# Optimization experiments

Hardware: AMD Instinct MI355X
Metric: run time of the kernel (lower is better)

## Reference

```python
import jax, jax.numpy as jnp
import numpy as np

B, T, D, H, DH, W = 2, 2048, 512, 8, 64, 64  # batch, seq, d_model, heads, d_head, window
BASE = 10000.0


def rope(x):
    # x: [b, t, d]; rotate-half RoPE applied over the full feature dim (as in source: pos_enc on d_model)
    d = x.shape[-1]
    half = d // 2
    inv_freq = BASE ** (-jnp.arange(half, dtype=jnp.float32) / half)          # [half]
    ang = jnp.arange(x.shape[1], dtype=jnp.float32)[:, None] * inv_freq       # [t, half]
    cos, sin = jnp.cos(ang), jnp.sin(ang)
    x1, x2 = x[..., :half], x[..., half:]
    return jnp.concatenate([x1 * cos - x2 * sin, x1 * sin + x2 * cos], axis=-1)


def setup_inputs() -> dict:
    key = jax.random.key(0)
    k0, k1, k2, k3 = jax.random.split(key, 4)
    x = jax.random.normal(k0, (B, T, D), jnp.float32)
    Wq = jax.random.normal(k1, (D, D), jnp.float32) / jnp.sqrt(D)
    Wkv = jax.random.normal(k2, (D, 2 * D), jnp.float32) / jnp.sqrt(D)
    # NOTE: source zero-inits lin; we use random weights so the output/grads are non-trivial
    Wlin = jax.random.normal(k3, (D, D), jnp.float32) / jnp.sqrt(D)
    blin = jnp.zeros((D,), jnp.float32)
    return {"x": x, "Wq": Wq, "Wkv": Wkv, "Wlin": Wlin, "blin": blin}


def reference(x, Wq, Wkv, Wlin, blin):
    b, t, _ = x.shape
    scale = DH ** -0.5
    q = rope(x @ Wq).reshape(b, t, H, DH).transpose(0, 2, 1, 3)               # [b,h,t,d]
    kv = x @ Wkv
    k, v = kv[..., :D], kv[..., D:]
    k = rope(k).reshape(b, t, H, DH).transpose(0, 2, 1, 3)                    # [b,h,t,d]
    v = v.reshape(b, t, H, DH).transpose(0, 2, 1, 3)                          # [b,h,t,d]
    pad = [(0, 0), (0, 0), (W - 1, 0), (0, 0)]
    kp, vp = jnp.pad(k, pad), jnp.pad(v, pad)                                 # [b,h,t+W-1,d]
    idx = jnp.arange(t)[:, None] + jnp.arange(W)[None, :]                     # [t,W] sliding-window gather
    kw, vw = kp[:, :, idx], vp[:, :, idx]                                     # [b,h,t,W,d]
    attn = jax.nn.softmax(jnp.einsum('bhtd,bhtwd->bhtw', q, kw) * scale, axis=-1)
    out = jnp.einsum('bhtw,bhtwd->bhtd', attn, vw)                            # [b,h,t,d]
    out = out.transpose(0, 2, 1, 3).reshape(b, t, D)
    return out @ Wlin + blin
```

## Files before the change

### kernel.cpp

```cpp
#include <hip/hip_runtime.h>
#include <cstddef>

#define T_N 2048
#define M_N 4096
#define KW  512

typedef __attribute__((ext_vector_type(4))) float f32x4;
typedef _Float16 f16x8 __attribute__((ext_vector_type(8)));
typedef _Float16 f16x4 __attribute__((ext_vector_type(4)));
typedef _Float16 f16x2 __attribute__((ext_vector_type(2)));

#define GLOAD_LDS(g, l) __builtin_amdgcn_global_load_lds( \
    (const __attribute__((address_space(1))) unsigned int*)(g), \
    (__attribute__((address_space(3))) unsigned int*)(l), 16, 0, 0)

__global__ __launch_bounds__(256) void prep(
    const float* __restrict__ x, const float* __restrict__ Wq,
    const float* __restrict__ Wkv, const float* __restrict__ Wlin,
    _Float16* __restrict__ Axp, _Float16* __restrict__ Wcatp,
    _Float16* __restrict__ Wlinp, _Float16* __restrict__ tab16) {
  __shared__ float tile[64][65];
  const int bid = blockIdx.x;
  const int tid = threadIdx.x;
  if (bid < 1024) {
    int idx = bid * 256 + tid;
    int m = idx >> 6, k8 = (idx & 63) << 3;
    const float* src = x + (size_t)m * 512 + k8;
    const float4 a = *(const float4*)src;
    const float4 b = *(const float4*)(src + 4);
    f16x8 o;
    o[0] = (_Float16)a.x; o[1] = (_Float16)a.y; o[2] = (_Float16)a.z; o[3] = (_Float16)a.w;
    o[4] = (_Float16)b.x; o[5] = (_Float16)b.y; o[6] = (_Float16)b.z; o[7] = (_Float16)b.w;
    *(f16x8*)(Axp + (size_t)m * 512 + k8) = o;
    return;
  }
  if (bid >= 1280) {
    int gid = (bid - 1280) * 256 + tid;
    int t = gid >> 8, f = gid & 255;
    float invf = exp2f(-0.05190512648261503f * (float)f);
    float s, c;
    sincosf((float)t * invf, &s, &c);
    f16x2 cs;
    cs[0] = (_Float16)c; cs[1] = (_Float16)s;
    *(f16x2*)(tab16 + 2 * ((size_t)t * 256 + f)) = cs;
    return;
  }
  int wb = bid - 1024;
  const float* W; int N; int mode; int bx, by;
  if (wb < 64)       { W = Wq;   N = 512;  mode = 0; bx = wb & 7;  by = wb >> 3; }
  else if (wb < 192) { wb -= 64;  W = Wkv; N = 1024; mode = 1; bx = wb & 15; by = wb >> 4; }
  else               { wb -= 192; W = Wlin; N = 512; mode = 2; bx = wb & 7;  by = wb >> 3; }
  const int n0 = bx * 64, k0 = by * 64;
#pragma unroll
  for (int it = 0; it < 16; ++it) {
    int idx = tid + it * 256;
    int r = idx >> 6, c = idx & 63;
    tile[r][c] = W[(size_t)(k0 + r) * N + n0 + c];
  }
  __syncthreads();
#pragma unroll
  for (int it = 0; it < 16; ++it) {
    int idx = tid + it * 256;
    int n = idx >> 6, kk = idx & 63;
    int cg = n0 + n;
    int np; _Float16* out;
    if (mode == 0)      { np = 2 * (cg & 255) + (cg >> 8); out = Wcatp; }
    else if (mode == 1) { np = (cg < 512) ? 512 + 2 * (cg & 255) + (cg >> 8)
                                          : 1024 + (cg - 512);
                          out = Wcatp; }
    else                { np = cg; out = Wlinp; }
    out[(size_t)np * KW + k0 + kk] = (_Float16)tile[kk][n];
  }
}

__global__ __launch_bounds__(256) void gemm_qkv_rope(
    const _Float16* __restrict__ Ap, const _Float16* __restrict__ Bp,
    const _Float16* __restrict__ tab16, _Float16* __restrict__ Qh,
    _Float16* __restrict__ Kh, _Float16* __restrict__ Vh) {
  __shared__ __align__(16) _Float16 sm[64 * 64 + 128 * 64];
  _Float16* sA = sm;
  _Float16* sB = sm + 64 * 64;
  const int tid = threadIdx.x;
  const int wid = tid >> 6, lane = tid & 63;
  const int il = lane & 15, g = lane >> 4;
  const int m0 = blockIdx.y * 64, n0 = blockIdx.x * 128;
  const int wm = (wid >> 1) * 32, wn = (wid & 1) * 64;
  f32x4 acc[2][4] = {};

  const _Float16* ga = Ap + (size_t)(m0 + wid * 16 + (lane >> 3)) * KW + (lane & 7) * 8;
  const _Float16* gb = Bp + (size_t)(n0 + wid * 32 + (lane >> 3)) * KW + (lane & 7) * 8;
  _Float16* la = sA + wid * 16 * 64;
  _Float16* lb = sB + wid * 32 * 64;

  for (int k0 = 0; k0 < KW; k0 += 64) {
    GLOAD_LDS(ga + k0, la);
    GLOAD_LDS(ga + 8 * KW + k0, la + 8 * 64);
#pragma unroll
    for (int p = 0; p < 4; ++p)
      GLOAD_LDS(gb + (size_t)(p * 8) * KW + k0, lb + p * 8 * 64);
    __syncthreads();
#pragma unroll
    for (int ks = 0; ks < 2; ++ks) {
      f16x8 af[2], bf[4];
#pragma unroll
      for (int i = 0; i < 2; ++i)
        af[i] = *(const f16x8*)&sA[(wm + i * 16 + il) * 64 + ks * 32 + g * 8];
#pragma unroll
      for (int j = 0; j < 4; ++j)
        bf[j] = *(const f16x8*)&sB[(wn + j * 16 + il) * 64 + ks * 32 + g * 8];
#pragma unroll
      for (int i = 0; i < 2; ++i)
#pragma unroll
        for (int j = 0; j < 4; ++j)
          acc[i][j] = __builtin_amdgcn_mfma_f32_16x16x32_f16(af[i], bf[j], acc[i][j], 0, 0, 0);
    }
    __syncthreads();
  }
  const int b8 = (m0 >> 11) * 8;
  const int tb = m0 & (T_N - 1);
  const bool isv = (n0 >= 1024);
  const bool isk = (n0 >= 512) && !isv;
  _Float16* OT  = sm;
  _Float16* OTV = sm;

  if (isv) {
#pragma unroll
    for (int i = 0; i < 2; ++i)
#pragma unroll
      for (int j = 0; j < 4; ++j) {
        f32x4 v = acc[i][j];
        int col = wn + 16 * j + il;
#pragma unroll
        for (int r = 0; r < 4; ++r) {
          int tl = wm + i * 16 + g * 4 + r;
          OTV[col * 72 + tl] = (_Float16)v[r];
        }
      }
    __syncthreads();
    const int cv = n0 - 1024;
#pragma unroll
    for (int it = 0; it < 4; ++it) {
      int c = tid + it * 256;
      int col = c >> 3, t8 = (c & 7) * 8;
      int h = (cv + col) >> 6, d = (cv + col) & 63;
      *(f16x8*)(Vh + ((size_t)(b8 + h) * 64 + d) * T_N + tb + t8) =
          *(const f16x8*)&OTV[col * 72 + t8];
    }
    return;
  }
  const int n0p = n0 - (isk ? 512 : 0);
  const int h0 = n0p >> 7;
#pragma unroll
  for (int i = 0; i < 2; ++i) {
#pragma unroll
    for (int j = 0; j < 4; ++j) {
      f32x4 v = acc[i][j];
#pragma unroll
      for (int r = 0; r < 4; ++r) {
        float self = v[r];
        float part = __shfl_xor(self, 1);
        int tl = wm + i * 16 + g * 4 + r;
        int tpos = tb + tl;
        int p = il & 1;
        int f = (n0p + wn + 16 * j + (il & 14)) >> 1;
        f16x2 cs = *(const f16x2*)(tab16 + 2 * ((size_t)tpos * 256 + f));
        float c = (float)cs[0], s = (float)cs[1];
        float o = p ? (self * c + part * s) : (self * c - part * s);
        OT[(p * 64 + tl) * 72 + (f & 63)] = (_Float16)o;
      }
    }
  }
  __syncthreads();
  _Float16* dst = isk ? Kh : Qh;
#pragma unroll
  for (int it = 0; it < 4; ++it) {
    int c = tid + it * 256;
    int p = c >> 9, row = (c >> 3) & 63, d8 = (c & 7) * 8;
    *(f16x8*)(dst + ((size_t)(b8 + h0 + 4 * p) * T_N + tb + row) * 64 + d8) =
        *(const f16x8*)&OT[(p * 64 + row) * 72 + d8];
  }
}

__global__ __launch_bounds__(256, 2) void attn_fused(
    const _Float16* __restrict__ Qh, const _Float16* __restrict__ Kh,
    const _Float16* __restrict__ Vh, _Float16* __restrict__ Aout) {
  __shared__ __align__(16) _Float16 sm[31232];
  _Float16* Ks  = sm;
  _Float16* VTs = sm + 9216;
  _Float16* Qs  = sm + 17920;
  _Float16* Ps  = sm + 22528;
  _Float16* OH  = sm;

  const int wgid = blockIdx.x;
  const int orig = (wgid & 7) * 64 + (wgid >> 3);
  const int tile = orig & 31;
  const int h = (orig >> 5) & 7;
  const int b = orig >> 8;
  const int t0 = tile * 64;
  const int tid = threadIdx.x;
  const size_t bh = (size_t)(b * 8 + h);

#pragma unroll
  for (int itn = 0; itn < 2; ++itn) {
    int c = tid + itn * 256;
    int row = c >> 3, d8 = (c & 7) * 8;
    *(f16x8*)(Qs + row * 72 + d8) =
        *(const f16x8*)(Qh + (bh * T_N + t0 + row) * 64 + d8);
  }
#pragma unroll
  for (int itn = 0; itn < 4; ++itn) {
    int c = tid + itn * 256;
    int jr = c >> 3, d8 = (c & 7) * 8;
    int p = t0 - 64 + jr;
    f16x8 o = {};
    if (p >= 0) o = *(const f16x8*)(Kh + (bh * T_N + p) * 64 + d8);
    *(f16x8*)(Ks + jr * 72 + d8) = o;
  }
#pragma unroll
  for (int itn = 0; itn < 4; ++itn) {
    int c = tid + itn * 256;
    int d = c & 63, jr8 = (c >> 6) * 8;
    int p8 = t0 - 64 + jr8;
    f16x8 o = {};
    if (p8 >= 0) o = *(const f16x8*)(Vh + (bh * 64 + d) * T_N + p8);
    *(f16x8*)(VTs + d * 136 + jr8) = o;
  }
  __syncthreads();

  const int lane = tid & 63;
  const int il = lane & 15, g = lane >> 4;
  const int it = tid >> 6;
  const int i_q = 16 * it + il;

  f32x4 sacc[5] = {};
  {
    f16x8 qf0 = *(const f16x8*)(Qs + i_q * 72 + 8 * g);
    f16x8 qf1 = *(const f16x8*)(Qs + i_q * 72 + 32 + 8 * g);
#pragma unroll
    for (int jt5 = 0; jt5 < 5; ++jt5) {
      int jrow = 16 * (it + jt5) + il;
      f16x8 a0 = *(const f16x8*)(Ks + jrow * 72 + 8 * g);
      f16x8 a1 = *(const f16x8*)(Ks + jrow * 72 + 32 + 8 * g);
      sacc[jt5] = __builtin_amdgcn_mfma_f32_16x16x32_f16(a0, qf0, sacc[jt5], 0, 0, 0);
      sacc[jt5] = __builtin_amdgcn_mfma_f32_16x16x32_f16(a1, qf1, sacc[jt5], 0, 0, 0);
    }
  }
  float mx = -3e38f;
#pragma unroll
  for (int jt5 = 0; jt5 < 5; ++jt5)
#pragma unroll
    for (int r = 0; r < 4; ++r) {
      int j = 16 * (it + jt5) + 4 * g + r;
      int wv = j - 1 - i_q;
      if (wv >= 0 && wv < 64) mx = fmaxf(mx, sacc[jt5][r]);
    }
  mx = fmaxf(mx, __shfl_xor(mx, 16));
  mx = fmaxf(mx, __shfl_xor(mx, 32));
  float sum = 0.f;
#pragma unroll
  for (int jt5 = 0; jt5 < 5; ++jt5) {
    f16x4 pv;
#pragma unroll
    for (int r = 0; r < 4; ++r) {
      int j = 16 * (it + jt5) + 4 * g + r;
      int wv = j - 1 - i_q;
      float ex = 0.f;
      if (wv >= 0 && wv < 64) {
        ex = exp2f((sacc[jt5][r] - mx) * 0.18033688011112042f);
        sum += ex;
      }
      pv[r] = (_Float16)ex;
    }
    *(f16x4*)(Ps + i_q * 136 + 16 * (it + jt5) + 4 * g) = pv;
  }
  sum += __shfl_xor(sum, 16);
  sum += __shfl_xor(sum, 32);
  {
    int jtz = (it & 1) ? (it - 1) : (it + 5);
    f16x4 z = {};
    *(f16x4*)(Ps + i_q * 136 + 16 * jtz + 4 * g) = z;
  }

  const int jb = 32 * (it >> 1);
  f32x4 oacc[4] = {};
#pragma unroll
  for (int ks = 0; ks < 3; ++ks) {
    f16x8 pf = *(const f16x8*)(Ps + i_q * 136 + jb + 32 * ks + 8 * g);
#pragma unroll
    for (int dt = 0; dt < 4; ++dt) {
      f16x8 vf = *(const f16x8*)(VTs + (16 * dt + il) * 136 + jb + 32 * ks + 8 * g);
      oacc[dt] = __builtin_amdgcn_mfma_f32_16x16x32_f16(pf, vf, oacc[dt], 0, 0, 0);
    }
  }
  __syncthreads();
#pragma unroll
  for (int r = 0; r < 4; ++r) {
    float s4 = __shfl(sum, 4 * g + r);
    float inv = 1.f / s4;
    int i = 16 * it + 4 * g + r;
#pragma unroll
    for (int dt = 0; dt < 4; ++dt) {
      int d = 16 * dt + il;
      OH[i * 72 + d] = (_Float16)(oacc[dt][r] * inv);
    }
  }
  __syncthreads();
#pragma unroll
  for (int itn = 0; itn < 2; ++itn) {
    int c = tid + itn * 256;
    int row = c >> 3, d8 = (c & 7) * 8;
    *(f16x8*)(Aout + ((size_t)(b * T_N + t0 + row)) * 512 + h * 64 + d8) =
        *(const f16x8*)(OH + row * 72 + d8);
  }
}

__global__ __launch_bounds__(256) void gemm_out(
    const _Float16* __restrict__ Ap, const _Float16* __restrict__ Bp,
    const float* __restrict__ bias, float* __restrict__ C) {
  __shared__ __align__(16) _Float16 sA[64 * 64];
  __shared__ __align__(16) _Float16 sB[64 * 64];
  const int tid = threadIdx.x;
  const int wid = tid >> 6, lane = tid & 63;
  const int il = lane & 15, g = lane >> 4;
  const int m0 = blockIdx.y * 64, n0 = blockIdx.x * 64;
  const int wm = (wid >> 1) * 32, wn = (wid & 1) * 32;
  f32x4 acc[2][2] = {};

  const _Float16* ga = Ap + (size_t)(m0 + wid * 16 + (lane >> 3)) * KW + (lane & 7) * 8;
  const _Float16* gb = Bp + (size_t)(n0 + wid * 16 + (lane >> 3)) * KW + (lane & 7) * 8;
  _Float16* la = sA + wid * 16 * 64;
  _Float16* lb = sB + wid * 16 * 64;

  for (int k0 = 0; k0 < KW; k0 += 64) {
    GLOAD_LDS(ga + k0, la);
    GLOAD_LDS(ga + 8 * KW + k0, la + 8 * 64);
    GLOAD_LDS(gb + k0, lb);
    GLOAD_LDS(gb + 8 * KW + k0, lb + 8 * 64);
    __syncthreads();
#pragma unroll
    for (int ks = 0; ks < 2; ++ks) {
      f16x8 af[2], bf[2];
#pragma unroll
      for (int i = 0; i < 2; ++i)
        af[i] = *(const f16x8*)&sA[(wm + i * 16 + il) * 64 + ks * 32 + g * 8];
#pragma unroll
      for (int j = 0; j < 2; ++j)
        bf[j] = *(const f16x8*)&sB[(wn + j * 16 + il) * 64 + ks * 32 + g * 8];
#pragma unroll
      for (int i = 0; i < 2; ++i)
#pragma unroll
        for (int j = 0; j < 2; ++j)
          acc[i][j] = __builtin_amdgcn_mfma_f32_16x16x32_f16(af[i], bf[j], acc[i][j], 0, 0, 0);
    }
    __syncthreads();
  }
  const int cn = n0 + wn + il;
  const int rbase = m0 + wm + g * 4;
#pragma unroll
  for (int j = 0; j < 2; ++j) {
    float badd = bias[cn + j * 16];
#pragma unroll
    for (int i = 0; i < 2; ++i)
#pragma unroll
      for (int r = 0; r < 4; ++r)
        C[(size_t)(rbase + i * 16 + r) * 512 + cn + j * 16] = acc[i][j][r] + badd;
  }
}

extern "C" void kernel_launch(void* const* d_in, const int* in_sizes, int n_in,
                              void* d_out, int out_size, void* d_ws, size_t ws_size,
                              hipStream_t stream) {
  const float* x    = (const float*)d_in[0];
  const float* Wq   = (const float*)d_in[1];
  const float* Wkv  = (const float*)d_in[2];
  const float* Wlin = (const float*)d_in[3];
  const float* blin = (const float*)d_in[4];
  float* out = (float*)d_out;

  char* ws = (char*)d_ws;
  _Float16* Axp   = (_Float16*)(ws);
  _Float16* Wcatp = (_Float16*)(ws + 4194304);
  _Float16* Wlinp = (_Float16*)(ws + 5767168);
  _Float16* tab16 = (_Float16*)(ws + 6291456);
  _Float16* Qh    = (_Float16*)(ws + 8388608);
  _Float16* Kh    = (_Float16*)(ws + 12582912);
  _Float16* Vh    = (_Float16*)(ws + 16777216);
  _Float16* Aaop  = (_Float16*)(ws + 20971520);

  prep<<<3328, 256, 0, stream>>>(x, Wq, Wkv, Wlin, Axp, Wcatp, Wlinp, tab16);
  gemm_qkv_rope<<<dim3(12, 64), 256, 0, stream>>>(Axp, Wcatp, tab16, Qh, Kh, Vh);
  attn_fused<<<512, 256, 0, stream>>>(Qh, Kh, Vh, Aaop);
  gemm_out<<<dim3(8, 64), 256, 0, stream>>>(Aaop, Wlinp, blin, out);
}
```

Before: 104.1 us.

## Fuse all four kernels into one persistent kernel with grid barriers

Merges the prep, QKV GEMM+RoPE, sliding-window attention and output GEMM kernels into a single 512-block persistent kernel. The stages are separated by software grid barriers built on atomic counters, and the counters are reset with a memset before each launch. This is meant to remove the launch overhead and inter-kernel gaps between the four stages. The cost is spin-wait barriers, a fixed 512-block grid that must all be co-resident or the kernel deadlocks, and a QKV GEMM stage that now spreads 768 tiles unevenly over 512 blocks.

After: 272.5 us. 162% more time.

```diff
diff --git a/kernel.cpp b/kernel.cpp
--- a/kernel.cpp
+++ b/kernel.cpp
@@ -4,6 +4,7 @@
 #define T_N 2048
 #define M_N 4096
 #define KW  512
+#define NBLK 512
 
 typedef __attribute__((ext_vector_type(4))) float f32x4;
 typedef _Float16 f16x8 __attribute__((ext_vector_type(8)));
@@ -14,356 +15,372 @@
     (const __attribute__((address_space(1))) unsigned int*)(g), \
     (__attribute__((address_space(3))) unsigned int*)(l), 16, 0, 0)
 
-__global__ __launch_bounds__(256) void prep(
+__device__ __forceinline__ void gridbar(unsigned* cnt) {
+  __syncthreads();
+  if (threadIdx.x == 0) {
+    __threadfence();
+    __hip_atomic_fetch_add(cnt, 1u, __ATOMIC_ACQ_REL, __HIP_MEMORY_SCOPE_AGENT);
+    while (__hip_atomic_load(cnt, __ATOMIC_ACQUIRE, __HIP_MEMORY_SCOPE_AGENT) < NBLK)
+      __builtin_amdgcn_s_sleep(2);
+    __threadfence();
+  }
+  __syncthreads();
+}
+
+__global__ __launch_bounds__(256, 2) void fused_all(
     const float* __restrict__ x, const float* __restrict__ Wq,
     const float* __restrict__ Wkv, const float* __restrict__ Wlin,
+    const float* __restrict__ blin, float* __restrict__ Cout,
     _Float16* __restrict__ Axp, _Float16* __restrict__ Wcatp,
-    _Float16* __restrict__ Wlinp, _Float16* __restrict__ tab16) {
-  __shared__ float tile[64][65];
+    _Float16* __restrict__ Wlinp, _Float16* __restrict__ tab16,
+    _Float16* __restrict__ Qh, _Float16* __restrict__ Kh,
+    _Float16* __restrict__ Vh, _Float16* __restrict__ Aaop,
+    unsigned* __restrict__ bar) {
+  __shared__ __align__(16) char smraw[62464];
   const int bid = blockIdx.x;
   const int tid = threadIdx.x;
-  if (bid < 1024) {
-    int idx = bid * 256 + tid;
-    int m = idx >> 6, k8 = (idx & 63) << 3;
-    const float* src = x + (size_t)m * 512 + k8;
-    const float4 a = *(const float4*)src;
-    const float4 b = *(const float4*)(src + 4);
-    f16x8 o;
-    o[0] = (_Float16)a.x; o[1] = (_Float16)a.y; o[2] = (_Float16)a.z; o[3] = (_Float16)a.w;
-    o[4] = (_Float16)b.x; o[5] = (_Float16)b.y; o[6] = (_Float16)b.z; o[7] = (_Float16)b.w;
-    *(f16x8*)(Axp + (size_t)m * 512 + k8) = o;
-    return;
+
+  {
+#pragma unroll
+    for (int itn = 0; itn < 2; ++itn) {
+      int idx = bid * 512 + itn * 256 + tid;
+      int m = idx >> 6, k8 = (idx & 63) << 3;
+      const float* src = x + (size_t)m * 512 + k8;
+      const float4 a = *(const float4*)src;
+      const float4 b = *(const float4*)(src + 4);
+      f16x8 o;
+      o[0] = (_Float16)a.x; o[1] = (_Float16)a.y; o[2] = (_Float16)a.z; o[3] = (_Float16)a.w;
+      o[4] = (_Float16)b.x; o[5] = (_Float16)b.y; o[6] = (_Float16)b.z; o[7] = (_Float16)b.w;
+      *(f16x8*)(Axp + (size_t)m * 512 + k8) = o;
+    }
+    if (bid < 256) {
+      float (*tile)[65] = (float(*)[65])smraw;
+      int wb = bid;
+      const float* W; int N; int mode; int bx, by;
+      if (wb < 64)       { W = Wq;   N = 512;  mode = 0; bx = wb & 7;  by = wb >> 3; }
+      else if (wb < 192) { wb -= 64;  W = Wkv; N = 1024; mode = 1; bx = wb & 15; by = wb >> 4; }
+      else               { wb -= 192; W = Wlin; N = 512; mode = 2; bx = wb & 7;  by = wb >> 3; }
+      const int n0 = bx * 64, k0 = by * 64;
+#pragma unroll
+      for (int itn = 0; itn < 16; ++itn) {
+        int idx = tid + itn * 256;
+        int r = idx >> 6, c = idx & 63;
+        tile[r][c] = W[(size_t)(k0 + r) * N + n0 + c];
+      }
+      __syncthreads();
+#pragma unroll
+      for (int itn = 0; itn < 16; ++itn) {
+        int idx = tid + itn * 256;
+        int n = idx >> 6, kk = idx & 63;
+        int cg = n0 + n;
+        int np; _Float16* outp;
+        if (mode == 0)      { np = 2 * (cg & 255) + (cg >> 8); outp = Wcatp; }
+        else if (mode == 1) { np = (cg < 512) ? 512 + 2 * (cg & 255) + (cg >> 8)
+                                              : 1024 + (cg - 512);
+                              outp = Wcatp; }
+        else                { np = cg; outp = Wlinp; }
+        outp[(size_t)np * KW + k0 + kk] = (_Float16)tile[kk][n];
+      }
+    } else {
+#pragma unroll
+      for (int itn = 0; itn < 8; ++itn) {
+        int gid = (bid - 256) * 2048 + itn * 256 + tid;
+        int t = gid >> 8, f = gid & 255;
+        float invf = exp2f(-0.05190512648261503f * (float)f);
+        float s, c;
+        sincosf((float)t * invf, &s, &c);
+        f16x2 cs;
+        cs[0] = (_Float16)c; cs[1] = (_Float16)s;
+        *(f16x2*)(tab16 + 2 * ((size_t)t * 256 + f)) = cs;
+      }
+    }
   }
-  if (bid >= 1280) {
-    int gid = (bid - 1280) * 256 + tid;
-    int t = gid >> 8, f = gid & 255;
-    float invf = exp2f(-0.05190512648261503f * (float)f);
-    float s, c;
-    sincosf((float)t * invf, &s, &c);
-    f16x2 cs;
-    cs[0] = (_Float16)c; cs[1] = (_Float16)s;
-    *(f16x2*)(tab16 + 2 * ((size_t)t * 256 + f)) = cs;
-    return;
+  gridbar(bar + 0);
+
+  for (int tt = bid; tt < 768; tt += NBLK) {
+    __syncthreads();
+    _Float16* sA = (_Float16*)smraw;
+    _Float16* sB = (_Float16*)smraw + 64 * 64;
+    const int wid = tid >> 6, lane = tid & 63;
+    const int il = lane & 15, g = lane >> 4;
+    const int m0 = (tt & 63) * 64, n0 = (tt >> 6) * 128;
+    const int wm = (wid >> 1) * 32, wn = (wid & 1) * 64;
+    f32x4 acc[2][4] = {};
+
+    const _Float16* ga = Axp + (size_t)(m0 + wid * 16 + (lane >> 3)) * KW + (lane & 7) * 8;
+    const _Float16* gb = Wcatp + (size_t)(n0 + wid * 32 + (lane >> 3)) * KW + (lane & 7) * 8;
+    _Float16* la = sA + wid * 16 * 64;
+    _Float16* lb = sB + wid * 32 * 64;
+
+    for (int k0 = 0; k0 < KW; k0 += 64) {
+      GLOAD_LDS(ga + k0, la);
+      GLOAD_LDS(ga + 8 * KW + k0, la + 8 * 64);
+#pragma unroll
+      for (int p = 0; p < 4; ++p)
+        GLOAD_LDS(gb + (size_t)(p * 8) * KW + k0, lb + p * 8 * 64);
+      __syncthreads();
+#pragma unroll
+      for (int ks = 0; ks < 2; ++ks) {
+        f16x8 af[2], bf[4];
+#pragma unroll
+        for (int i = 0; i < 2; ++i)
+          af[i] = *(const f16x8*)&sA[(wm + i * 16 + il) * 64 + ks * 32 + g * 8];
+#pragma unroll
+        for (int j = 0; j < 4; ++j)
+          bf[j] = *(const f16x8*)&sB[(wn + j * 16 + il) * 64 + ks * 32 + g * 8];
+#pragma unroll
+        for (int i = 0; i < 2; ++i)
+#pragma unroll
+          for (int j = 0; j < 4; ++j)
+            acc[i][j] = __builtin_amdgcn_mfma_f32_16x16x32_f16(af[i], bf[j], acc[i][j], 0, 0, 0);
+      }
+      __syncthreads();
+    }
+    const int b8 = (m0 >> 11) * 8;
+    const int tb = m0 & (T_N - 1);
+    const bool isv = (n0 >= 1024);
+    const bool isk = (n0 >= 512) && !isv;
+    _Float16* OT  = (_Float16*)smraw;
+    _Float16* OTV = (_Float16*)smraw;
+
+    if (isv) {
+#pragma unroll
+      for (int i = 0; i < 2; ++i)
+#pragma unroll
+        for (int j = 0; j < 4; ++j) {
+          f32x4 v = acc[i][j];
+          int col = wn + 16 * j + il;
+#pragma unroll
+          for (int r = 0; r < 4; ++r) {
+            int tl = wm + i * 16 + g * 4 + r;
+            OTV[col * 72 + tl] = (_Float16)v[r];
+          }
+        }
+      __syncthreads();
+      const int cv = n0 - 1024;
+#pragma unroll
+      for (int itn = 0; itn < 4; ++itn) {
+        int c = tid + itn * 256;
+        int col = c >> 3, t8 = (c & 7) * 8;
+        int h = (cv + col) >> 6, d = (cv + col) & 63;
+        *(f16x8*)(Vh + ((size_t)(b8 + h) * 64 + d) * T_N + tb + t8) =
+            *(const f16x8*)&OTV[col * 72 + t8];
+      }
+    } else {
+      const int n0p = n0 - (isk ? 512 : 0);
+      const int h0 = n0p >> 7;
+#pragma unroll
+      for (int i = 0; i < 2; ++i) {
+#pragma unroll
+        for (int j = 0; j < 4; ++j) {
+          f32x4 v = acc[i][j];
+#pragma unroll
+          for (int r = 0; r < 4; ++r) {
+            float self = v[r];
+            float part = __shfl_xor(self, 1);
+            int tl = wm + i * 16 + g * 4 + r;
+            int tpos = tb + tl;
+            int p = il & 1;
+            int f = (n0p + wn + 16 * j + (il & 14)) >> 1;
+            f16x2 cs = *(const f16x2*)(tab16 + 2 * ((size_t)tpos * 256 + f));
+            float c = (float)cs[0], s = (float)cs[1];
+            float o = p ? (self * c + part * s) : (self * c - part * s);
+            OT[(p * 64 + tl) * 72 + (f & 63)] = (_Float16)o;
+          }
+        }
+      }
+      __syncthreads();
+      _Float16* dst = isk ? Kh : Qh;
+#pragma unroll
+      for (int itn = 0; itn < 4; ++itn) {
+        int c = tid + itn * 256;
+        int p = c >> 9, row = (c >> 3) & 63, d8 = (c & 7) * 8;
+        *(f16x8*)(dst + ((size_t)(b8 + h0 + 4 * p) * T_N + tb + row) * 64 + d8) =
+            *(const f16x8*)&OT[(p * 64 + row) * 72 + d8];
+      }
+    }
   }
-  int wb = bid - 1024;
-  const float* W; int N; int mode; int bx, by;
-  if (wb < 64)       { W = Wq;   N = 512;  mode = 0; bx = wb & 7;  by = wb >> 3; }
-  else if (wb < 192) { wb -= 64;  W = Wkv; N = 1024; mode = 1; bx = wb & 15; by = wb >> 4; }
-  else               { wb -= 192; W = Wlin; N = 512; mode = 2; bx = wb & 7;  by = wb >> 3; }
-  const int n0 = bx * 64, k0 = by * 64;
-#pragma unroll
-  for (int it = 0; it < 16; ++it) {
-    int idx = tid + it * 256;
-    int r = idx >> 6, c = idx & 63;
-    tile[r][c] = W[(size_t)(k0 + r) * N + n0 + c];
+  gridbar(bar + 1);
+
+  {
+    __syncthreads();
+    _Float16* sm16 = (_Float16*)smraw;
+    _Float16* Ks  = sm16;
+    _Float16* VTs = sm16 + 9216;
+    _Float16* Qs  = sm16 + 17920;
+    _Float16* Ps  = sm16 + 22528;
+    _Float16* OH  = sm16;
+
+    const int orig = (bid & 7) * 64 + (bid >> 3);
+    const int tile = orig & 31;
+    const int h = (orig >> 5) & 7;
+    const int b = orig >> 8;
+    const int t0 = tile * 64;
+    const size_t bh = (size_t)(b * 8 + h);
+
+#pragma unroll
+    for (int itn = 0; itn < 2; ++itn) {
+      int c = tid + itn * 256;
+      int row = c >> 3, d8 = (c & 7) * 8;
+      *(f16x8*)(Qs + row * 72 + d8) =
+          *(const f16x8*)(Qh + (bh * T_N + t0 + row) * 64 + d8);
+    }
+#pragma unroll
+    for (int itn = 0; itn < 4; ++itn) {
+      int c = tid + itn * 256;
+      int jr = c >> 3, d8 = (c & 7) * 8;
+      int p = t0 - 64 + jr;
+      f16x8 o = {};
+      if (p >= 0) o = *(const f16x8*)(Kh + (bh * T_N + p) * 64 + d8);
+      *(f16x8*)(Ks + jr * 72 + d8) = o;
+    }
+#pragma unroll
+    for (int itn = 0; itn < 4; ++itn) {
+      int c = tid + itn * 256;
+      int d = c & 63, jr8 = (c >> 6) * 8;
+      int p8 = t0 - 64 + jr8;
+      f16x8 o = {};
+      if (p8 >= 0) o = *(const f16x8*)(Vh + (bh * 64 + d) * T_N + p8);
+      *(f16x8*)(VTs + d * 136 + jr8) = o;
+    }
+    __syncthreads();
+
+    const int lane = tid & 63;
+    const int il = lane & 15, g = lane >> 4;
+    const int it = tid >> 6;
+    const int i_q = 16 * it + il;
+
+    f32x4 sacc[5] = {};
+    {
+      f16x8 qf0 = *(const f16x8*)(Qs + i_q * 72 + 8 * g);
+      f16x8 qf1 = *(const f16x8*)(Qs + i_q * 72 + 32 + 8 * g);
+#pragma unroll
+      for (int jt5 = 0; jt5 < 5; ++jt5) {
+        int jrow = 16 * (it + jt5) + il;
+        f16x8 a0 = *(const f16x8*)(Ks + jrow * 72 + 8 * g);
+        f16x8 a1 = *(const f16x8*)(Ks + jrow * 72 + 32 + 8 * g);
+        sacc[jt5] = __builtin_amdgcn_mfma_f32_16x16x32_f16(a0, qf0, sacc[jt5], 0, 0, 0);
+        sacc[jt5] = __builtin_amdgcn_mfma_f32_16x16x32_f16(a1, qf1, sacc[jt5], 0, 0, 0);
+      }
+    }
+    float mx = -3e38f;
+#pragma unroll
+    for (int jt5 = 0; jt5 < 5; ++jt5)
+#pragma unroll
+      for (int r = 0; r < 4; ++r) {
+        int j = 16 * (it + jt5) + 4 * g + r;
+        int wv = j - 1 - i_q;
+        if (wv >= 0 && wv < 64) mx = fmaxf(mx, sacc[jt5][r]);
+      }
+    mx = fmaxf(mx, __shfl_xor(mx, 16));
+    mx = fmaxf(mx, __shfl_xor(mx, 32));
+    float sum = 0.f;
+#pragma unroll
+    for (int jt5 = 0; jt5 < 5; ++jt5) {
+      f16x4 pv;
+#pragma unroll
+      for (int r = 0; r < 4; ++r) {
+        int j = 16 * (it + jt5) + 4 * g + r;
+        int wv = j - 1 - i_q;
+        float ex = 0.f;
+        if (wv >= 0 && wv < 64) {
+          ex = exp2f((sacc[jt5][r] - mx) * 0.18033688011112042f);
+          sum += ex;
+        }
+        pv[r] = (_Float16)ex;
+      }
+      *(f16x4*)(Ps + i_q * 136 + 16 * (it + jt5) + 4 * g) = pv;
+    }
+    sum += __shfl_xor(sum, 16);
+    sum += __shfl_xor(sum, 32);
+    {
+      int jtz = (it & 1) ? (it - 1) : (it + 5);
+      f16x4 z = {};
+      *(f16x4*)(Ps + i_q * 136 + 16 * jtz + 4 * g) = z;
+    }
+    const int jb = 32 * (it >> 1);
+    f32x4 oacc[4] = {};
+#pragma unroll
+    for (int ks = 0; ks < 3; ++ks) {
+      f16x8 pf = *(const f16x8*)(Ps + i_q * 136 + jb + 32 * ks + 8 * g);
+#pragma unroll
+      for (int dt = 0; dt < 4; ++dt) {
+        f16x8 vf = *(const f16x8*)(VTs + (16 * dt + il) * 136 + jb + 32 * ks + 8 * g);
+        oacc[dt] = __builtin_amdgcn_mfma_f32_16x16x32_f16(pf, vf, oacc[dt], 0, 0, 0);
+      }
+    }
+    __syncthreads();
+#pragma unroll
+    for (int r = 0; r < 4; ++r) {
+      float s4 = __shfl(sum, 4 * g + r);
+      float inv = 1.f / s4;
+      int i = 16 * it + 4 * g + r;
+#pragma unroll
+      for (int dt = 0; dt < 4; ++dt) {
+        int d = 16 * dt + il;
+        OH[i * 72 + d] = (_Float16)(oacc[dt][r] * inv);
+      }
+    }
+    __syncthreads();
+#pragma unroll
+    for (int itn = 0; itn < 2; ++itn) {
+      int c = tid + itn * 256;
+      int row = c >> 3, d8 = (c & 7) * 8;
+      *(f16x8*)(Aaop + ((size_t)(b * T_N + t0 + row)) * 512 + h * 64 + d8) =
+          *(const f16x8*)(OH + row * 72 + d8);
+    }
   }
-  __syncthreads();
-#pragma unroll
-  for (int it = 0; it < 16; ++it) {
-    int idx = tid + it * 256;
-    int n = idx >> 6, kk = idx & 63;
-    int cg = n0 + n;
-    int np; _Float16* out;
-    if (mode == 0)      { np = 2 * (cg & 255) + (cg >> 8); out = Wcatp; }
-    else if (mode == 1) { np = (cg < 512) ? 512 + 2 * (cg & 255) + (cg >> 8)
-                                          : 1024 + (cg - 512);
-                          out = Wcatp; }
-    else                { np = cg; out = Wlinp; }
-    out[(size_t)np * KW + k0 + kk] = (_Float16)tile[kk][n];
-  }
-}
-
-__global__ __launch_bounds__(256) void gemm_qkv_rope(
-    const _Float16* __restrict__ Ap, const _Float16* __restrict__ Bp,
-    const _Float16* __restrict__ tab16, _Float16* __restrict__ Qh,
-    _Float16* __restrict__ Kh, _Float16* __restrict__ Vh) {
-  __shared__ __align__(16) _Float16 sm[64 * 64 + 128 * 64];
-  _Float16* sA = sm;
-  _Float16* sB = sm + 64 * 64;
-  const int tid = threadIdx.x;
-  const int wid = tid >> 6, lane = tid & 63;
-  const int il = lane & 15, g = lane >> 4;
-  const int m0 = blockIdx.y * 64, n0 = blockIdx.x * 128;
-  const int wm = (wid >> 1) * 32, wn = (wid & 1) * 64;
-  f32x4 acc[2][4] = {};
-
-  const _Float16* ga = Ap + (size_t)(m0 + wid * 16 + (lane >> 3)) * KW + (lane & 7) * 8;
-  const _Float16* gb = Bp + (size_t)(n0 + wid * 32 + (lane >> 3)) * KW + (lane & 7) * 8;
-  _Float16* la = sA + wid * 16 * 64;
-  _Float16* lb = sB + wid * 32 * 64;
-
-  for (int k0 = 0; k0 < KW; k0 += 64) {
-    GLOAD_LDS(ga + k0, la);
-    GLOAD_LDS(ga + 8 * KW + k0, la + 8 * 64);
-#pragma unroll
-    for (int p = 0; p < 4; ++p)
-      GLOAD_LDS(gb + (size_t)(p * 8) * KW + k0, lb + p * 8 * 64);
-    __syncthreads();
-#pragma unroll
-    for (int ks = 0; ks < 2; ++ks) {
-      f16x8 af[2], bf[4];
+  gridbar(bar + 2);
+
+  {
+    __syncthreads();
+    _Float16* sA = (_Float16*)smraw;
+    _Float16* sB = (_Float16*)smraw + 64 * 64;
+    const int wid = tid >> 6, lane = tid & 63;
+    const int il = lane & 15, g = lane >> 4;
+    const int m0 = (bid >> 3) * 64, n0 = (bid & 7) * 64;
+    const int wm = (wid >> 1) * 32, wn = (wid & 1) * 32;
+    f32x4 acc[2][2] = {};
+
+    const _Float16* ga = Aaop + (size_t)(m0 + wid * 16 + (lane >> 3)) * KW + (lane & 7) * 8;
+    const _Float16* gb = Wlinp + (size_t)(n0 + wid * 16 + (lane >> 3)) * KW + (lane & 7) * 8;
+    _Float16* la = sA + wid * 16 * 64;
+    _Float16* lb = sB + wid * 16 * 64;
+
+    for (int k0 = 0; k0 < KW; k0 += 64) {
+      GLOAD_LDS(ga + k0, la);
+      GLOAD_LDS(ga + 8 * KW + k0, la + 8 * 64);
+      GLOAD_LDS(gb + k0, lb);
+      GLOAD_LDS(gb + 8 * KW + k0, lb + 8 * 64);
+      __syncthreads();
+#pragma unroll
+      for (int ks = 0; ks < 2; ++ks) {
+        f16x8 af[2], bf[2];
+#pragma unroll
+        for (int i = 0; i < 2; ++i)
+          af[i] = *(const f16x8*)&sA[(wm + i * 16 + il) * 64 + ks * 32 + g * 8];
+#pragma unroll
+        for (int j = 0; j < 2; ++j)
+          bf[j] = *(const f16x8*)&sB[(wn + j * 16 + il) * 64 + ks * 32 + g * 8];
+#pragma unroll
+        for (int i = 0; i < 2; ++i)
+#pragma unroll
+          for (int j = 0; j < 2; ++j)
+            acc[i][j] = __builtin_amdgcn_mfma_f32_16x16x32_f16(af[i], bf[j], acc[i][j], 0, 0, 0);
+      }
+      __syncthreads();
+    }
+    const int cn = n0 + wn + il;
+    const int rbase = m0 + wm + g * 4;
+#pragma unroll
+    for (int j = 0; j < 2; ++j) {
+      float badd = blin[cn + j * 16];
 #pragma unroll
       for (int i = 0; i < 2; ++i)
-        af[i] = *(const f16x8*)&sA[(wm + i * 16 + il) * 64 + ks * 32 + g * 8];
-#pragma unroll
-      for (int j = 0; j < 4; ++j)
-        bf[j] = *(const f16x8*)&sB[(wn + j * 16 + il) * 64 + ks * 32 + g * 8];
-#pragma unroll
-      for (int i = 0; i < 2; ++i)
-#pragma unroll
-        for (int j = 0; j < 4; ++j)
-          acc[i][j] = __builtin_amdgcn_mfma_f32_16x16x32_f16(af[i], bf[j], acc[i][j], 0, 0, 0);
-    }
-    __syncthreads();
-  }
-  const int b8 = (m0 >> 11) * 8;
-  const int tb = m0 & (T_N - 1);
-  const bool isv = (n0 >= 1024);
-  const bool isk = (n0 >= 512) && !isv;
-  _Float16* OT  = sm;
-  _Float16* OTV = sm;
-
-  if (isv) {
-#pragma unroll
-    for (int i = 0; i < 2; ++i)
-#pragma unroll
-      for (int j = 0; j < 4; ++j) {
-        f32x4 v = acc[i][j];
-        int col = wn + 16 * j + il;
-#pragma unroll
-        for (int r = 0; r < 4; ++r) {
-          int tl = wm + i * 16 + g * 4 + r;
-          OTV[col * 72 + tl] = (_Float16)v[r];
-        }
-      }
-    __syncthreads();
-    const int cv = n0 - 1024;
-#pragma unroll
-    for (int it = 0; it < 4; ++it) {
-      int c = tid + it * 256;
-      int col = c >> 3, t8 = (c & 7) * 8;
-      int h = (cv + col) >> 6, d = (cv + col) & 63;
-      *(f16x8*)(Vh + ((size_t)(b8 + h) * 64 + d) * T_N + tb + t8) =
-          *(const f16x8*)&OTV[col * 72 + t8];
-    }
-    return;
-  }
-  const int n0p = n0 - (isk ? 512 : 0);
-  const int h0 = n0p >> 7;
-#pragma unroll
-  for (int i = 0; i < 2; ++i) {
-#pragma unroll
-    for (int j = 0; j < 4; ++j) {
-      f32x4 v = acc[i][j];
-#pragma unroll
-      for (int r = 0; r < 4; ++r) {
-        float self = v[r];
-        float part = __shfl_xor(self, 1);
-        int tl = wm + i * 16 + g * 4 + r;
-        int tpos = tb + tl;
-        int p = il & 1;
-        int f = (n0p + wn + 16 * j + (il & 14)) >> 1;
-        f16x2 cs = *(const f16x2*)(tab16 + 2 * ((size_t)tpos * 256 + f));
-        float c = (float)cs[0], s = (float)cs[1];
-        float o = p ? (self * c + part * s) : (self * c - part * s);
-        OT[(p * 64 + tl) * 72 + (f & 63)] = (_Float16)o;
-      }
-    }
-  }
-  __syncthreads();
-  _Float16* dst = isk ? Kh : Qh;
-#pragma unroll
-  for (int it = 0; it < 4; ++it) {
-    int c = tid + it * 256;
-    int p = c >> 9, row = (c >> 3) & 63, d8 = (c & 7) * 8;
-    *(f16x8*)(dst + ((size_t)(b8 + h0 + 4 * p) * T_N + tb + row) * 64 + d8) =
-        *(const f16x8*)&OT[(p * 64 + row) * 72 + d8];
-  }
-}
-
-__global__ __launch_bounds__(256, 2) void attn_fused(
-    const _Float16* __restrict__ Qh, const _Float16* __restrict__ Kh,
-    const _Float16* __restrict__ Vh, _Float16* __restrict__ Aout) {
-  __shared__ __align__(16) _Float16 sm[31232];
-  _Float16* Ks  = sm;
-  _Float16* VTs = sm + 9216;
-  _Float16* Qs  = sm + 17920;
-  _Float16* Ps  = sm + 22528;
-  _Float16* OH  = sm;
-
-  const int wgid = blockIdx.x;
-  const int orig = (wgid & 7) * 64 + (wgid >> 3);
-  const int tile = orig & 31;
-  const int h = (orig >> 5) & 7;
-  const int b = orig >> 8;
-  const int t0 = tile * 64;
-  const int tid = threadIdx.x;
-  const size_t bh = (size_t)(b * 8 + h);
-
-#pragma unroll
-  for (int itn = 0; itn < 2; ++itn) {
-    int c = tid + itn * 256;
-    int row = c >> 3, d8 = (c & 7) * 8;
-    *(f16x8*)(Qs + row * 72 + d8) =
-        *(const f16x8*)(Qh + (bh * T_N + t0 + row) * 64 + d8);
-  }
-#pragma unroll
-  for (int itn = 0; itn < 4; ++itn) {
-    int c = tid + itn * 256;
-    int jr = c >> 3, d8 = (c & 7) * 8;
-    int p = t0 - 64 + jr;
-    f16x8 o = {};
-    if (p >= 0) o = *(const f16x8*)(Kh + (bh * T_N + p) * 64 + d8);
-    *(f16x8*)(Ks + jr * 72 + d8) = o;
-  }
-#pragma unroll
-  for (int itn = 0; itn < 4; ++itn) {
-    int c = tid + itn * 256;
-    int d = c & 63, jr8 = (c >> 6) * 8;
-    int p8 = t0 - 64 + jr8;
-    f16x8 o = {};
-    if (p8 >= 0) o = *(const f16x8*)(Vh + (bh * 64 + d) * T_N + p8);
-    *(f16x8*)(VTs + d * 136 + jr8) = o;
-  }
-  __syncthreads();
-
-  const int lane = tid & 63;
-  const int il = lane & 15, g = lane >> 4;
-  const int it = tid >> 6;
-  const int i_q = 16 * it + il;
-
-  f32x4 sacc[5] = {};
-  {
-    f16x8 qf0 = *(const f16x8*)(Qs + i_q * 72 + 8 * g);
-    f16x8 qf1 = *(const f16x8*)(Qs + i_q * 72 + 32 + 8 * g);
-#pragma unroll
-    for (int jt5 = 0; jt5 < 5; ++jt5) {
-      int jrow = 16 * (it + jt5) + il;
-      f16x8 a0 = *(const f16x8*)(Ks + jrow * 72 + 8 * g);
-      f16x8 a1 = *(const f16x8*)(Ks + jrow * 72 + 32 + 8 * g);
-      sacc[jt5] = __builtin_amdgcn_mfma_f32_16x16x32_f16(a0, qf0, sacc[jt5], 0, 0, 0);
-      sacc[jt5] = __builtin_amdgcn_mfma_f32_16x16x32_f16(a1, qf1, sacc[jt5], 0, 0, 0);
-    }
-  }
-  float mx = -3e38f;
-#pragma unroll
-  for (int jt5 = 0; jt5 < 5; ++jt5)
-#pragma unroll
-    for (int r = 0; r < 4; ++r) {
-      int j = 16 * (it + jt5) + 4 * g + r;
-      int wv = j - 1 - i_q;
-      if (wv >= 0 && wv < 64) mx = fmaxf(mx, sacc[jt5][r]);
-    }
-  mx = fmaxf(mx, __shfl_xor(mx, 16));
-  mx = fmaxf(mx, __shfl_xor(mx, 32));
-  float sum = 0.f;
-#pragma unroll
-  for (int jt5 = 0; jt5 < 5; ++jt5) {
-    f16x4 pv;
-#pragma unroll
-    for (int r = 0; r < 4; ++r) {
-      int j = 16 * (it + jt5) + 4 * g + r;
-      int wv = j - 1 - i_q;
-      float ex = 0.f;
-      if (wv >= 0 && wv < 64) {
-        ex = exp2f((sacc[jt5][r] - mx) * 0.18033688011112042f);
-        sum += ex;
-      }
-      pv[r] = (_Float16)ex;
-    }
-    *(f16x4*)(Ps + i_q * 136 + 16 * (it + jt5) + 4 * g) = pv;
-  }
-  sum += __shfl_xor(sum, 16);
-  sum += __shfl_xor(sum, 32);
-  {
-    int jtz = (it & 1) ? (it - 1) : (it + 5);
-    f16x4 z = {};
-    *(f16x4*)(Ps + i_q * 136 + 16 * jtz + 4 * g) = z;
-  }
-
-  const int jb = 32 * (it >> 1);
-  f32x4 oacc[4] = {};
-#pragma unroll
-  for (int ks = 0; ks < 3; ++ks) {
-    f16x8 pf = *(const f16x8*)(Ps + i_q * 136 + jb + 32 * ks + 8 * g);
-#pragma unroll
-    for (int dt = 0; dt < 4; ++dt) {
-      f16x8 vf = *(const f16x8*)(VTs + (16 * dt + il) * 136 + jb + 32 * ks + 8 * g);
-      oacc[dt] = __builtin_amdgcn_mfma_f32_16x16x32_f16(pf, vf, oacc[dt], 0, 0, 0);
-    }
-  }
-  __syncthreads();
-#pragma unroll
-  for (int r = 0; r < 4; ++r) {
-    float s4 = __shfl(sum, 4 * g + r);
-    float inv = 1.f / s4;
-    int i = 16 * it + 4 * g + r;
-#pragma unroll
-    for (int dt = 0; dt < 4; ++dt) {
-      int d = 16 * dt + il;
-      OH[i * 72 + d] = (_Float16)(oacc[dt][r] * inv);
-    }
-  }
-  __syncthreads();
-#pragma unroll
-  for (int itn = 0; itn < 2; ++itn) {
-    int c = tid + itn * 256;
-    int row = c >> 3, d8 = (c & 7) * 8;
-    *(f16x8*)(Aout + ((size_t)(b * T_N + t0 + row)) * 512 + h * 64 + d8) =
-        *(const f16x8*)(OH + row * 72 + d8);
-  }
-}
-
-__global__ __launch_bounds__(256) void gemm_out(
-    const _Float16* __restrict__ Ap, const _Float16* __restrict__ Bp,
-    const float* __restrict__ bias, float* __restrict__ C) {
-  __shared__ __align__(16) _Float16 sA[64 * 64];
-  __shared__ __align__(16) _Float16 sB[64 * 64];
-  const int tid = threadIdx.x;
-  const int wid = tid >> 6, lane = tid & 63;
-  const int il = lane & 15, g = lane >> 4;
-  const int m0 = blockIdx.y * 64, n0 = blockIdx.x * 64;
-  const int wm = (wid >> 1) * 32, wn = (wid & 1) * 32;
-  f32x4 acc[2][2] = {};
-
-  const _Float16* ga = Ap + (size_t)(m0 + wid * 16 + (lane >> 3)) * KW + (lane & 7) * 8;
-  const _Float16* gb = Bp + (size_t)(n0 + wid * 16 + (lane >> 3)) * KW + (lane & 7) * 8;
-  _Float16* la = sA + wid * 16 * 64;
-  _Float16* lb = sB + wid * 16 * 64;
-
-  for (int k0 = 0; k0 < KW; k0 += 64) {
-    GLOAD_LDS(ga + k0, la);
-    GLOAD_LDS(ga + 8 * KW + k0, la + 8 * 64);
-    GLOAD_LDS(gb + k0, lb);
-    GLOAD_LDS(gb + 8 * KW + k0, lb + 8 * 64);
-    __syncthreads();
-#pragma unroll
-    for (int ks = 0; ks < 2; ++ks) {
-      f16x8 af[2], bf[2];
-#pragma unroll
-      for (int i = 0; i < 2; ++i)
-        af[i] = *(const f16x8*)&sA[(wm + i * 16 + il) * 64 + ks * 32 + g * 8];
-#pragma unroll
-      for (int j = 0; j < 2; ++j)
-        bf[j] = *(const f16x8*)&sB[(wn + j * 16 + il) * 64 + ks * 32 + g * 8];
-#pragma unroll
-      for (int i = 0; i < 2; ++i)
-#pragma unroll
-        for (int j = 0; j < 2; ++j)
-          acc[i][j] = __builtin_amdgcn_mfma_f32_16x16x32_f16(af[i], bf[j], acc[i][j], 0, 0, 0);
-    }
-    __syncthreads();
-  }
-  const int cn = n0 + wn + il;
-  const int rbase = m0 + wm + g * 4;
-#pragma unroll
-  for (int j = 0; j < 2; ++j) {
-    float badd = bias[cn + j * 16];
-#pragma unroll
-    for (int i = 0; i < 2; ++i)
-#pragma unroll
-      for (int r = 0; r < 4; ++r)
-        C[(size_t)(rbase + i * 16 + r) * 512 + cn + j * 16] = acc[i][j][r] + badd;
+#pragma unroll
+        for (int r = 0; r < 4; ++r)
+          Cout[(size_t)(rbase + i * 16 + r) * 512 + cn + j * 16] = acc[i][j][r] + badd;
+    }
   }
 }
 
@@ -386,9 +403,10 @@
   _Float16* Kh    = (_Float16*)(ws + 12582912);
   _Float16* Vh    = (_Float16*)(ws + 16777216);
   _Float16* Aaop  = (_Float16*)(ws + 20971520);
-
-  prep<<<3328, 256, 0, stream>>>(x, Wq, Wkv, Wlin, Axp, Wcatp, Wlinp, tab16);
-  gemm_qkv_rope<<<dim3(12, 64), 256, 0, stream>>>(Axp, Wcatp, tab16, Qh, Kh, Vh);
-  attn_fused<<<512, 256, 0, stream>>>(Qh, Kh, Vh, Aaop);
-  gemm_out<<<dim3(8, 64), 256, 0, stream>>>(Aaop, Wlinp, blin, out);
+  unsigned* bar   = (unsigned*)(ws + 25165824);
+
+  hipMemsetAsync(bar, 0, 64, stream);
+  fused_all<<<NBLK, 256, 0, stream>>>(x, Wq, Wkv, Wlin, blin, out,
+                                      Axp, Wcatp, Wlinp, tab16,
+                                      Qh, Kh, Vh, Aaop, bar);
 }
```
